# Kernel optimization log

Hardware: AMD Instinct MI355X
Metric: run time of the kernel (lower is better)

## Reference

```python
import jax, jax.numpy as jnp
import numpy as np

B, T, D, H = 512, 512, 128, 64


def _lstm(x, Wih, Whh, b):
    """Single-layer batch-first LSTM, PyTorch gate order (i, f, g, o).
    x: [B, T, Din]; Wih: [4Hc, Din]; Whh: [4Hc, Hc]; b: [4Hc] (= b_ih + b_hh).
    Returns (outputs [B, T, Hc], final_hidden [B, Hc]).
    """
    Hc = Whh.shape[1]
    Bn = x.shape[0]
    # Precompute input projections for all timesteps: [B, T, 4Hc]
    xp = jnp.einsum('bti,gi->btg', x, Wih) + b

    def step(carry, xt):
        h, c = carry
        g = xt + h @ Whh.T                      # [B, 4Hc]
        i = jax.nn.sigmoid(g[:, :Hc])
        f = jax.nn.sigmoid(g[:, Hc:2 * Hc])
        gg = jnp.tanh(g[:, 2 * Hc:3 * Hc])
        o = jax.nn.sigmoid(g[:, 3 * Hc:])
        c = f * c + i * gg
        h = o * jnp.tanh(c)
        return (h, c), h

    init = (jnp.zeros((Bn, Hc), x.dtype), jnp.zeros((Bn, Hc), x.dtype))
    (h_last, _), ys = jax.lax.scan(step, init, jnp.swapaxes(xp, 0, 1))
    return jnp.swapaxes(ys, 0, 1), h_last


def setup_inputs() -> dict:
    key = jax.random.key(0)
    ks = jax.random.split(key, 7)
    se = 1.0 / np.sqrt(H)   # PyTorch LSTM init scale (encoder, hidden=H)
    sd = 1.0 / np.sqrt(D)   # decoder, hidden=D
    return {
        'x': jax.random.normal(ks[0], (B, T, D), jnp.float32),
        'Wih_e': jax.random.uniform(ks[1], (4 * H, D), jnp.float32, -se, se),
        'Whh_e': jax.random.uniform(ks[2], (4 * H, H), jnp.float32, -se, se),
        'b_e': jax.random.uniform(ks[3], (4 * H,), jnp.float32, -se, se),
        'Wih_d': jax.random.uniform(ks[4], (4 * D, H), jnp.float32, -sd, sd),
        'Whh_d': jax.random.uniform(ks[5], (4 * D, D), jnp.float32, -sd, sd),
        'b_d': jax.random.uniform(ks[6], (4 * D,), jnp.float32, -sd, sd),
    }


def reference(x, Wih_e, Whh_e, b_e, Wih_d, Whh_d, b_d):
    # Encoder: take final hidden state [B, H]
    _, h = _lstm(x, Wih_e, Whh_e, b_e)
    # hidden.repeat(T,1,1).permute(1,0,2) -> tile across time: [B, T, H]
    hrep = jnp.broadcast_to(h[:, None, :], (h.shape[0], x.shape[1], h.shape[1]))
    # Decoder: full output sequence [B, T, D]
    reconstructed, _ = _lstm(hrep, Wih_d, Whh_d, b_d)
    return reconstructed
```

## Files before the change

kernel.cpp:

```cpp
#include <hip/hip_runtime.h>

#define TT 512

typedef float f32x2 __attribute__((ext_vector_type(2)));
typedef float f32x4 __attribute__((ext_vector_type(4)));

template<int CTRL>
__device__ __forceinline__ float dpp_mov(float v) {
    return __int_as_float(__builtin_amdgcn_mov_dpp(__float_as_int(v), CTRL, 0xF, 0xF, true));
}
__device__ __forceinline__ float swz_xor4(float v) {
    return __int_as_float(__builtin_amdgcn_ds_swizzle(__float_as_int(v), 0x101F));
}
__device__ __forceinline__ void pk(f32x2& a, f32x2 w, f32x2 v) {
    asm("v_pk_fma_f32 %0, %1, %2, %0" : "+v"(a) : "v"(w), "v"(v));
}

__device__ __forceinline__ float merge8(float* s) {
    s[0] += dpp_mov<0xB1>(s[4]);
    s[1] += dpp_mov<0xB1>(s[5]);
    s[2] += dpp_mov<0xB1>(s[6]);
    s[3] += dpp_mov<0xB1>(s[7]);
    s[0] += dpp_mov<0x4E>(s[2]);
    s[1] += dpp_mov<0x4E>(s[3]);
    return s[0] + swz_xor4(s[1]);
}

__global__ __launch_bounds__(1024, 4)
void dec_kernel(const float* __restrict__ h_enc,
                const float* __restrict__ Wih,
                const float* __restrict__ Whh,
                const float* __restrict__ bias,
                float* __restrict__ out)
{
    const int tid = threadIdx.x;
    const int gg  = tid >> 3;
    const int q   = tid & 7;
    const int q0 = q & 1, q1 = (q >> 1) & 1, q2 = (q >> 2) & 1;
    const int msk2 = (q0 << 1) | q1;
    const int b0  = blockIdx.x * 2;

    __shared__ __align__(16) float he[2][64];
    __shared__ __align__(16) float hb[2][2 * 160];

    if (tid < 128) he[tid >> 6][tid & 63] = h_enc[(size_t)(b0 + (tid >> 6)) * 64 + (tid & 63)];
    if (tid < 256) {
        int r = tid >> 7, j = tid & 127;
        hb[0][r * 160 + j + 4 * (j >> 4)] = 0.f;
    }

    f32x4 w[4][4];
    #pragma unroll
    for (int m = 0; m < 4; ++m) {
        const float* src = Whh + (size_t)((m ^ msk2) * 128 + gg) * 128 + 16 * q;
        #pragma unroll
        for (int c = 0; c < 4; ++c) w[m][c] = *(const f32x4*)(src + 4 * c);
    }

    const int t4own = 2 * q0 + q1;
    const float sA = (t4own == 2) ? 2.f : 1.f;
    const float sC = (t4own == 2) ? -1.f : 0.f;
    const bool writer = (q0 == 0) && (q1 == 0);
    const int rr  = q2;
    const int oA  = q2 * 160;
    const int oB  = (q2 ^ 1) * 160;
    const int kres = 20 * q;
    const int pwj = q2 * 160 + gg + 4 * (gg >> 4);

    __syncthreads();

    float xp;
    {
        const float* heA = he[q2] + 8 * q;
        const float* heB = he[q2 ^ 1] + 8 * q;
        f32x4 hA0 = *(const f32x4*)heA, hA1 = *(const f32x4*)(heA + 4);
        f32x4 hB0 = *(const f32x4*)heB, hB1 = *(const f32x4*)(heB + 4);
        float s[8];
        #pragma unroll
        for (int m = 0; m < 4; ++m) {
            const float* ws = Wih + (size_t)((m ^ msk2) * 128 + gg) * 64 + 8 * q;
            f32x4 w0 = *(const f32x4*)ws, w1 = *(const f32x4*)(ws + 4);
            f32x2 aA = {0.f, 0.f}, aB = {0.f, 0.f};
            pk(aA, w0.lo, hA0.lo); pk(aA, w0.hi, hA0.hi);
            pk(aA, w1.lo, hA1.lo); pk(aA, w1.hi, hA1.hi);
            pk(aB, w0.lo, hB0.lo); pk(aB, w0.hi, hB0.hi);
            pk(aB, w1.lo, hB1.lo); pk(aB, w1.hi, hB1.hi);
            s[2 * m]     = aA.x + aA.y;
            s[2 * m + 1] = aB.x + aB.y;
        }
        xp = merge8(s) + bias[t4own * 128 + gg];
    }

    float c_state = 0.f;
    size_t optr = ((size_t)(b0 + rr) * TT) * 128 + gg;

#define DSTEP(CUR, NXT) {                                                      \
    const float* bAp = (CUR) + oA + kres;                                      \
    const float* bBp = (CUR) + oB + kres;                                      \
    f32x4 ch[4]; f32x2 accA[4], accB[4];                                       \
    _Pragma("unroll") for (int c = 0; c < 4; ++c) ch[c] = *(const f32x4*)(bAp + 4 * c); \
    _Pragma("unroll") for (int m = 0; m < 4; ++m) { f32x2 z2 = {0.f, 0.f};     \
        _Pragma("unroll") for (int c = 0; c < 4; ++c) { pk(z2, w[m][c].lo, ch[c].lo); pk(z2, w[m][c].hi, ch[c].hi); } \
        accA[m] = z2; }                                                        \
    _Pragma("unroll") for (int c = 0; c < 4; ++c) ch[c] = *(const f32x4*)(bBp + 4 * c); \
    _Pragma("unroll") for (int m = 0; m < 4; ++m) { f32x2 z2 = {0.f, 0.f};     \
        _Pragma("unroll") for (int c = 0; c < 4; ++c) { pk(z2, w[m][c].lo, ch[c].lo); pk(z2, w[m][c].hi, ch[c].hi); } \
        accB[m] = z2; }                                                        \
    float s[8];                                                                \
    _Pragma("unroll") for (int m = 0; m < 4; ++m) {                            \
        s[2 * m] = accA[m].x + accA[m].y; s[2 * m + 1] = accB[m].x + accB[m].y; } \
    float z = merge8(s) + xp;                                                  \
    float ez = __expf(-z * sA);                                                \
    float v  = fmaf(__builtin_amdgcn_rcpf(1.0f + ez), sA, sC);                 \
    float vi = dpp_mov<0x00>(v); float vg = dpp_mov<0x55>(v);                  \
    float vf = dpp_mov<0xAA>(v); float vo = dpp_mov<0xFF>(v);                  \
    c_state = fmaf(vf, c_state, vi * vg);                                      \
    float e2 = __expf(-2.f * c_state);                                         \
    float hv = vo * fmaf(__builtin_amdgcn_rcpf(1.f + e2), 2.f, -1.f);          \
    if (writer) { (NXT)[pwj] = hv; out[optr] = hv; }                           \
    optr += 128;                                                               \
    __syncthreads(); }

    #pragma unroll 1
    for (int t = 0; t < TT; t += 2) {
        DSTEP(hb[0], hb[1]);
        DSTEP(hb[1], hb[0]);
    }
#undef DSTEP
}

__global__ __launch_bounds__(512, 2)
void enc_kernel(const float* __restrict__ x,
                const float* __restrict__ Wih,
                const float* __restrict__ Whh,
                const float* __restrict__ bias,
                float* __restrict__ h_out)
{
    const int tid = threadIdx.x;
    const int gg  = tid >> 3;
    const int q   = tid & 7;
    const int q0 = q & 1, q1 = (q >> 1) & 1, q2 = (q >> 2) & 1;
    const int msk2 = (q0 << 1) | q1;
    const int b0  = blockIdx.x * 2;

    __shared__ __align__(16) float xh[2][2 * 224];

    f32x4 w[4][6];
    #pragma unroll
    for (int m = 0; m < 4; ++m) {
        int row = (m ^ msk2) * 64 + gg;
        #pragma unroll
        for (int c = 0; c < 6; ++c) {
            int k0 = 24 * q + 4 * c;
            const float* src = (k0 < 128) ? (Wih + (size_t)row * 128 + k0)
                                          : (Whh + (size_t)row * 64 + (k0 - 128));
            w[m][c] = *(const f32x4*)src;
        }
    }

    const int t4own = 2 * q0 + q1;
    const float sA = (t4own == 2) ? 2.f : 1.f;
    const float sC = (t4own == 2) ? -1.f : 0.f;
    const bool writer = (q0 == 0) && (q1 == 0);
    const int rr  = q2;
    const int oA  = q2 * 224;
    const int oB  = (q2 ^ 1) * 224;
    const int kres = 28 * q;
    const int hj  = 128 + gg;
    const int pwj = q2 * 224 + hj + 4 * (hj / 24);
    const float xpc = bias[t4own * 64 + gg];

    const bool stager = (tid < 64);
    const int sr = (tid >> 5) & 1, sc = tid & 31;
    const int psl = sr * 224 + 4 * sc + 4 * ((4 * sc) / 24);
    const float* xbase = x + ((size_t)(b0 + sr) * TT) * 128 + 4 * sc;

    if (stager) *(f32x4*)(&xh[0][psl]) = *(const f32x4*)xbase;
    if (tid < 128) {
        int r = tid >> 6, j = 128 + (tid & 63);
        xh[0][r * 224 + j + 4 * (j / 24)] = 0.f;
    }

    float c_state = 0.f;
    float h_last = 0.f;
    __syncthreads();

#define ESTEP(CUR, NXT, T) {                                                   \
    f32x4 xnext;                                                               \
    if (stager) { int tl = (T) + 1 < TT ? (T) + 1 : TT - 1;                    \
        xnext = *(const f32x4*)(xbase + (size_t)tl * 128); }                   \
    const float* bAp = (CUR) + oA + kres;                                      \
    const float* bBp = (CUR) + oB + kres;                                      \
    f32x4 ch[6]; f32x2 accA[4], accB[4];                                       \
    _Pragma("unroll") for (int c = 0; c < 6; ++c) ch[c] = *(const f32x4*)(bAp + 4 * c); \
    _Pragma("unroll") for (int m = 0; m < 4; ++m) { f32x2 z2 = {0.f, 0.f};     \
        _Pragma("unroll") for (int c = 0; c < 6; ++c) { pk(z2, w[m][c].lo, ch[c].lo); pk(z2, w[m][c].hi, ch[c].hi); } \
        accA[m] = z2; }                                                        \
    _Pragma("unroll") for (int c = 0; c < 6; ++c) ch[c] = *(const f32x4*)(bBp + 4 * c); \
    _Pragma("unroll") for (int m = 0; m < 4; ++m) { f32x2 z2 = {0.f, 0.f};     \
        _Pragma("unroll") for (int c = 0; c < 6; ++c) { pk(z2, w[m][c].lo, ch[c].lo); pk(z2, w[m][c].hi, ch[c].hi); } \
        accB[m] = z2; }                                                        \
    float s[8];                                                                \
    _Pragma("unroll") for (int m = 0; m < 4; ++m) {                            \
        s[2 * m] = accA[m].x + accA[m].y; s[2 * m + 1] = accB[m].x + accB[m].y; } \
    float z = merge8(s) + xpc;                                                 \
    float ez = __expf(-z * sA);                                                \
    float v  = fmaf(__builtin_amdgcn_rcpf(1.0f + ez), sA, sC);                 \
    float vi = dpp_mov<0x00>(v); float vg = dpp_mov<0x55>(v);                  \
    float vf = dpp_mov<0xAA>(v); float vo = dpp_mov<0xFF>(v);                  \
    c_state = fmaf(vf, c_state, vi * vg);                                      \
    float e2 = __expf(-2.f * c_state);                                         \
    float hv = vo * fmaf(__builtin_amdgcn_rcpf(1.f + e2), 2.f, -1.f);          \
    h_last = hv;                                                               \
    if (writer) (NXT)[pwj] = hv;                                               \
    if (stager) *(f32x4*)((NXT) + psl) = xnext;                                \
    __syncthreads(); }

    #pragma unroll 1
    for (int t = 0; t < TT; t += 2) {
        ESTEP(xh[0], xh[1], t);
        ESTEP(xh[1], xh[0], t + 1);
    }
#undef ESTEP

    if (writer) h_out[(size_t)(b0 + rr) * 64 + gg] = h_last;
}

extern "C" void kernel_launch(void* const* d_in, const int* in_sizes, int n_in,
                              void* d_out, int out_size, void* d_ws, size_t ws_size,
                              hipStream_t stream) {
    const float* x     = (const float*)d_in[0];
    const float* Wih_e = (const float*)d_in[1];
    const float* Whh_e = (const float*)d_in[2];
    const float* b_e   = (const float*)d_in[3];
    const float* Wih_d = (const float*)d_in[4];
    const float* Whh_d = (const float*)d_in[5];
    const float* b_d   = (const float*)d_in[6];
    float* out   = (float*)d_out;
    float* h_enc = (float*)d_ws;

    enc_kernel<<<dim3(256), dim3(512), 0, stream>>>(x, Wih_e, Whh_e, b_e, h_enc);
    dec_kernel<<<dim3(256), dim3(1024), 0, stream>>>(h_enc, Wih_d, Whh_d, b_d, out);
}
```

Baseline: 1.051 ms.

## Split encoder K-reduction across 16 lanes per gate row with 1024 threads

The encoder kernel now uses 1024 threads per block, with 16 lanes cooperating on each hidden unit instead of 8. Each lane holds half as many weights (12 K-elements instead of 24) and does half the FMAs per step. A deeper swizzle reduction merges the partial sums. The padded shared-memory layout is dropped for a plain 192-stride buffer. This shortens the per-step serial dependency chain in the latency-bound recurrence, at the cost of an extra reduction stage, more waves syncing per barrier, and possible LDS bank conflicts from the unpadded layout.

Measured after the change: 1.120 ms. 1.06x slower.

```diff
diff --git a/kernel.cpp b/kernel.cpp
--- a/kernel.cpp
+++ b/kernel.cpp
@@ -11,6 +11,9 @@
 }
 __device__ __forceinline__ float swz_xor4(float v) {
     return __int_as_float(__builtin_amdgcn_ds_swizzle(__float_as_int(v), 0x101F));
+}
+__device__ __forceinline__ float swz_xor8(float v) {
+    return __int_as_float(__builtin_amdgcn_ds_swizzle(__float_as_int(v), 0x201F));
 }
 __device__ __forceinline__ void pk(f32x2& a, f32x2 w, f32x2 v) {
     asm("v_pk_fma_f32 %0, %1, %2, %0" : "+v"(a) : "v"(w), "v"(v));
@@ -129,7 +132,7 @@
 #undef DSTEP
 }
 
-__global__ __launch_bounds__(512, 2)
+__global__ __launch_bounds__(1024, 4)
 void enc_kernel(const float* __restrict__ x,
                 const float* __restrict__ Wih,
                 const float* __restrict__ Whh,
@@ -137,48 +140,47 @@
                 float* __restrict__ h_out)
 {
     const int tid = threadIdx.x;
-    const int gg  = tid >> 3;
-    const int q   = tid & 7;
-    const int q0 = q & 1, q1 = (q >> 1) & 1, q2 = (q >> 2) & 1;
+    const int gg  = tid >> 4;
+    const int q   = tid & 15;
+    const int q0 = q & 1, q1 = (q >> 1) & 1, q3 = (q >> 3) & 1;
     const int msk2 = (q0 << 1) | q1;
     const int b0  = blockIdx.x * 2;
 
-    __shared__ __align__(16) float xh[2][2 * 224];
-
-    f32x4 w[4][6];
+    __shared__ __align__(16) float xh[2][2 * 192];
+
+    f32x4 w[4][3];
     #pragma unroll
     for (int m = 0; m < 4; ++m) {
         int row = (m ^ msk2) * 64 + gg;
         #pragma unroll
-        for (int c = 0; c < 6; ++c) {
-            int k0 = 24 * q + 4 * c;
+        for (int c = 0; c < 3; ++c) {
+            int k0 = 12 * q + 4 * c;
             const float* src = (k0 < 128) ? (Wih + (size_t)row * 128 + k0)
                                           : (Whh + (size_t)row * 64 + (k0 - 128));
             w[m][c] = *(const f32x4*)src;
         }
     }
 
-    const int t4own = 2 * q0 + q1;
+    const int t4own = msk2;
     const float sA = (t4own == 2) ? 2.f : 1.f;
     const float sC = (t4own == 2) ? -1.f : 0.f;
-    const bool writer = (q0 == 0) && (q1 == 0);
-    const int rr  = q2;
-    const int oA  = q2 * 224;
-    const int oB  = (q2 ^ 1) * 224;
-    const int kres = 28 * q;
-    const int hj  = 128 + gg;
-    const int pwj = q2 * 224 + hj + 4 * (hj / 24);
+    const bool writer = ((q & 7) == 0);
+    const int rr  = q3;
+    const int oA  = q3 * 192;
+    const int oB  = (q3 ^ 1) * 192;
+    const int kres = 12 * q;
+    const int pwj = q3 * 192 + 128 + gg;
     const float xpc = bias[t4own * 64 + gg];
 
     const bool stager = (tid < 64);
     const int sr = (tid >> 5) & 1, sc = tid & 31;
-    const int psl = sr * 224 + 4 * sc + 4 * ((4 * sc) / 24);
+    const int psl = sr * 192 + 4 * sc;
     const float* xbase = x + ((size_t)(b0 + sr) * TT) * 128 + 4 * sc;
 
     if (stager) *(f32x4*)(&xh[0][psl]) = *(const f32x4*)xbase;
     if (tid < 128) {
-        int r = tid >> 6, j = 128 + (tid & 63);
-        xh[0][r * 224 + j + 4 * (j / 24)] = 0.f;
+        int r = tid >> 6, j = tid & 63;
+        xh[0][r * 192 + 128 + j] = 0.f;
     }
 
     float c_state = 0.f;
@@ -191,19 +193,29 @@
         xnext = *(const f32x4*)(xbase + (size_t)tl * 128); }                   \
     const float* bAp = (CUR) + oA + kres;                                      \
     const float* bBp = (CUR) + oB + kres;                                      \
-    f32x4 ch[6]; f32x2 accA[4], accB[4];                                       \
-    _Pragma("unroll") for (int c = 0; c < 6; ++c) ch[c] = *(const f32x4*)(bAp + 4 * c); \
-    _Pragma("unroll") for (int m = 0; m < 4; ++m) { f32x2 z2 = {0.f, 0.f};     \
-        _Pragma("unroll") for (int c = 0; c < 6; ++c) { pk(z2, w[m][c].lo, ch[c].lo); pk(z2, w[m][c].hi, ch[c].hi); } \
+    f32x4 ch[3]; f32x2 accA[4], accB[4];                                       \
+    _Pragma("unroll") for (int c = 0; c < 3; ++c) ch[c] = *(const f32x4*)(bAp + 4 * c); \
+    _Pragma("unroll") for (int m = 0; m < 4; ++m) { f32x2 z2 = {0.f, 0.f};     \
+        _Pragma("unroll") for (int c = 0; c < 3; ++c) { pk(z2, w[m][c].lo, ch[c].lo); pk(z2, w[m][c].hi, ch[c].hi); } \
         accA[m] = z2; }                                                        \
-    _Pragma("unroll") for (int c = 0; c < 6; ++c) ch[c] = *(const f32x4*)(bBp + 4 * c); \
-    _Pragma("unroll") for (int m = 0; m < 4; ++m) { f32x2 z2 = {0.f, 0.f};     \
-        _Pragma("unroll") for (int c = 0; c < 6; ++c) { pk(z2, w[m][c].lo, ch[c].lo); pk(z2, w[m][c].hi, ch[c].hi); } \
+    _Pragma("unroll") for (int c = 0; c < 3; ++c) ch[c] = *(const f32x4*)(bBp + 4 * c); \
+    _Pragma("unroll") for (int m = 0; m < 4; ++m) { f32x2 z2 = {0.f, 0.f};     \
+        _Pragma("unroll") for (int c = 0; c < 3; ++c) { pk(z2, w[m][c].lo, ch[c].lo); pk(z2, w[m][c].hi, ch[c].hi); } \
         accB[m] = z2; }                                                        \
     float s[8];                                                                \
     _Pragma("unroll") for (int m = 0; m < 4; ++m) {                            \
         s[2 * m] = accA[m].x + accA[m].y; s[2 * m + 1] = accB[m].x + accB[m].y; } \
-    float z = merge8(s) + xpc;                                                 \
+    \
+    \
+    s[0] += dpp_mov<0xB1>(s[4]);                                               \
+    s[1] += dpp_mov<0xB1>(s[5]);                                               \
+    s[2] += dpp_mov<0xB1>(s[6]);                                               \
+    s[3] += dpp_mov<0xB1>(s[7]);                                               \
+    s[0] += dpp_mov<0x4E>(s[2]);                                               \
+    s[1] += dpp_mov<0x4E>(s[3]);                                               \
+    s[0] += swz_xor4(s[0]);                                                    \
+    s[1] += swz_xor4(s[1]);                                                    \
+    float z = s[0] + swz_xor8(s[1]) + xpc;                                     \
     float ez = __expf(-z * sA);                                                \
     float v  = fmaf(__builtin_amdgcn_rcpf(1.0f + ez), sA, sC);                 \
     float vi = dpp_mov<0x00>(v); float vg = dpp_mov<0x55>(v);                  \
@@ -239,6 +251,6 @@
     float* out   = (float*)d_out;
     float* h_enc = (float*)d_ws;
 
-    enc_kernel<<<dim3(256), dim3(512), 0, stream>>>(x, Wih_e, Whh_e, b_e, h_enc);
+    enc_kernel<<<dim3(256), dim3(1024), 0, stream>>>(x, Wih_e, Whh_e, b_e, h_enc);
     dec_kernel<<<dim3(256), dim3(1024), 0, stream>>>(h_enc, Wih_d, Whh_d, b_d, out);
 }
```
